# Kernel tuning notes

Measured on AMD Instinct MI355X. Metric: run time of the kernel, lower is better.

## Reference

```python
import jax, jax.numpy as jnp
import numpy as np

B, L, D = 2, 1024, 768
K = 64            # window_size
MLP_HIDDEN = 128
DIFF_STEPS = 1
EPS = 1e-8        # torch F.cosine_similarity eps


def setup_inputs() -> dict:
    key = jax.random.key(0)
    ks = jax.random.split(key, 7)
    x = jax.random.normal(ks[0], (B, L, D), dtype=jnp.float32)
    alpha = jnp.asarray(0.1, dtype=jnp.float32)
    pos_emb = jax.random.normal(ks[1], (K, D), dtype=jnp.float32) * 0.02
    w1 = jax.random.normal(ks[2], (2 * D, MLP_HIDDEN), dtype=jnp.float32) * 0.02
    b1 = jnp.zeros((MLP_HIDDEN,), dtype=jnp.float32)
    w2 = jax.random.normal(ks[3], (MLP_HIDDEN, D), dtype=jnp.float32) * 0.02
    b2 = jnp.zeros((D,), dtype=jnp.float32)
    return {"x": x, "alpha": alpha, "pos_emb": pos_emb,
            "w1": w1, "b1": b1, "w2": w2, "b2": b2}


def reference(x, alpha, pos_emb, w1, b1, w2, b2):
    Bx, Lx, Dx = x.shape
    W = Lx - K + 1  # number of sliding windows
    # gather indices for unfold(2, K, 1): window w covers positions [w, w+K)
    idx = jnp.arange(W)[:, None] + jnp.arange(K)[None, :]  # [W, K]

    x_curr = x
    first_pre_energy = jnp.asarray(0.0, jnp.float32)
    final_post_energy = jnp.asarray(0.0, jnp.float32)
    total_update_norm = jnp.asarray(0.0, jnp.float32)
    total_cos_sim = jnp.asarray(0.0, jnp.float32)

    for step in range(DIFF_STEPS):
        windows = x_curr[:, idx, :]                 # [B, W, K, D]
        context = windows[:, :, :-1, :]             # [B, W, K-1, D]
        current = windows[:, :, -1, :]              # [B, W, D]
        pe = jnp.broadcast_to(pos_emb[: K - 1], (Bx, W, K - 1, Dx))
        mlp_in = jnp.concatenate([context, pe], axis=-1)        # [B, W, K-1, 2D]
        h = jax.nn.relu(jnp.einsum('bwkc,ch->bwkh', mlp_in, w1) + b1)
        pred = jnp.einsum('bwkh,hd->bwkd', h, w2) + b2          # [B, W, K-1, D]
        deltas = current[:, :, None, :] - pred                  # [B, W, K-1, D]
        mean_delta = deltas.mean(axis=2)                        # [B, W, D]
        update = -(alpha * mean_delta)                          # [B, W, D]
        x_next = x_curr.at[:, K - 1:, :].add(update)

        pre_energy = (mean_delta ** 2).sum(axis=-1).mean()
        up_norm = jnp.linalg.norm(update, axis=-1).mean()
        a = current
        b = current + update
        na = jnp.maximum(jnp.linalg.norm(a, axis=-1), EPS)
        nb = jnp.maximum(jnp.linalg.norm(b, axis=-1), EPS)
        cos_sim = ((a * b).sum(axis=-1) / (na * nb)).mean()

        if step == 0:
            first_pre_energy = pre_energy
        total_update_norm = total_update_norm + up_norm
        total_cos_sim = total_cos_sim + cos_sim
        x_curr = x_next
        alpha_val = jax.lax.stop_gradient(alpha)  # mirrors .item() detach
        post_energy = (1.0 - alpha_val) ** 2 * pre_energy
        if step == DIFF_STEPS - 1:
            final_post_energy = post_energy

    return (x_curr,
            first_pre_energy,
            final_post_energy,
            total_update_norm / DIFF_STEPS,
            total_cos_sim / DIFF_STEPS)
```

## Files before the change

kernel.cpp:

```cpp
#include <hip/hip_runtime.h>

constexpr int Bn = 2;
constexpr int Ln = 1024;
constexpr int Dn = 768;
constexpr int Hn = 128;
constexpr int KM1 = 63;
constexpr int Wn = 961;
constexpr int RB = 8;
constexpr int WB = 8;
constexpr int WCHUNKS = (Wn + WB - 1) / WB;
constexpr int NROW = Bn * Wn;
constexpr float EPSf = 1e-8f;

__device__ __forceinline__ float4 f4l(const float* p) { return *reinterpret_cast<const float4*>(p); }
__device__ __forceinline__ void f4s(float* p, float4 v) { *reinterpret_cast<float4*>(p) = v; }
__device__ __forceinline__ float4 f4fma(float s, float4 w, float4 a) {
    a.x = fmaf(s, w.x, a.x); a.y = fmaf(s, w.y, a.y);
    a.z = fmaf(s, w.z, a.z); a.w = fmaf(s, w.w, a.w);
    return a;
}

__global__ __launch_bounds__(1024)
void k_gemm1(const float* __restrict__ x, const float* __restrict__ pos_emb,
             const float* __restrict__ w1, const float* __restrict__ b1,
             float* __restrict__ xw1, float* __restrict__ pew1,
             float* __restrict__ out)
{
    __shared__ float xs[RB * Dn];
    __shared__ float part[8 * RB * Hn];
    const int tid = threadIdx.x;
    const int h4 = tid & 31;
    const int is = (tid >> 5) & 3;
    const int ks = tid >> 7;
    const int blk = blockIdx.x;
    constexpr int NXB = (Bn * Ln) / RB;
    const bool isX = blk < NXB;
    const int peb = blk - NXB;

    const float* src = isX ? (x + blk * RB * Dn) : (pos_emb + peb * RB * Dn);
    const int nv = isX ? RB : min(RB, KM1 - peb * RB);

    for (int idx = tid; idx < nv * (Dn / 4); idx += 1024)
        ((float4*)xs)[idx] = ((const float4*)src)[idx];
    __syncthreads();

    if (isX) {
        const int r0 = blk * RB;
        if ((r0 & (Ln - 1)) < KM1) {
            for (int idx = tid; idx < RB * (Dn / 4); idx += 1024) {
                const int i = idx / (Dn / 4);
                const int r = r0 + i;
                if ((r & (Ln - 1)) < KM1)
                    ((float4*)out)[r * (Dn / 4) + (idx - i * (Dn / 4))] = ((const float4*)xs)[idx];
            }
        }
    }

    const int woff = isX ? 0 : Dn;
    const int i0 = is * 2;
    float4 acc0 = make_float4(0.f, 0.f, 0.f, 0.f);
    float4 acc1 = acc0;
    const int cbase = ks * (Dn / 8);
    for (int cc = 0; cc < Dn / 8; cc += 4) {
        const int c = cbase + cc;
        const float* wp = w1 + (woff + c) * Hn + 4 * h4;
        const float4 wv0 = f4l(wp);
        const float4 wv1 = f4l(wp + Hn);
        const float4 wv2 = f4l(wp + 2 * Hn);
        const float4 wv3 = f4l(wp + 3 * Hn);
        const float4 x0 = ((const float4*)xs)[(i0 * Dn + c) >> 2];
        const float4 x1 = ((const float4*)xs)[((i0 + 1) * Dn + c) >> 2];
        acc0 = f4fma(x0.x, wv0, acc0); acc0 = f4fma(x0.y, wv1, acc0);
        acc0 = f4fma(x0.z, wv2, acc0); acc0 = f4fma(x0.w, wv3, acc0);
        acc1 = f4fma(x1.x, wv0, acc1); acc1 = f4fma(x1.y, wv1, acc1);
        acc1 = f4fma(x1.z, wv2, acc1); acc1 = f4fma(x1.w, wv3, acc1);
    }
    ((float4*)part)[((ks * RB + i0) * Hn + 4 * h4) >> 2] = acc0;
    ((float4*)part)[((ks * RB + i0 + 1) * Hn + 4 * h4) >> 2] = acc1;
    __syncthreads();

    const int oi = tid >> 7;
    const int oh = tid & 127;
    float s = 0.f;
    #pragma unroll
    for (int k2 = 0; k2 < 8; ++k2)
        s += part[(k2 * RB + oi) * Hn + oh];
    if (isX) {
        xw1[(blk * RB + oi) * Hn + oh] = s;
    } else if (oi < nv) {
        pew1[(peb * RB + oi) * Hn + oh] = s + b1[oh];
    }
}

__global__ __launch_bounds__(256)
void k_hbar(const float* __restrict__ xw1, const float* __restrict__ pew1,
            float* __restrict__ hbar)
{
    __shared__ float4 prt[8][32];
    const int tid = threadIdx.x;
    const int h4 = tid & 31;
    const int kg = tid >> 5;
    const int b = blockIdx.x / Wn;
    const int w = blockIdx.x - b * Wn;
    const float* xp = xw1 + (b * Ln + w + kg * 8) * Hn + 4 * h4;
    const float* pp = pew1 + (kg * 8) * Hn + 4 * h4;
    const int nk = (kg == 7) ? 7 : 8;
    float4 s = make_float4(0.f, 0.f, 0.f, 0.f);
    for (int j = 0; j < nk; ++j) {
        const float4 xv = f4l(xp + j * Hn);
        const float4 pv = f4l(pp + j * Hn);
        s.x += fmaxf(xv.x + pv.x, 0.f);
        s.y += fmaxf(xv.y + pv.y, 0.f);
        s.z += fmaxf(xv.z + pv.z, 0.f);
        s.w += fmaxf(xv.w + pv.w, 0.f);
    }
    prt[kg][h4] = s;
    __syncthreads();
    if (tid < 32) {
        float4 t = prt[0][tid];
        #pragma unroll
        for (int k = 1; k < 8; ++k) {
            const float4 u = prt[k][tid];
            t.x += u.x; t.y += u.y; t.z += u.z; t.w += u.w;
        }
        const float sc = 1.0f / 63.0f;
        t.x *= sc; t.y *= sc; t.z *= sc; t.w *= sc;
        ((float4*)(hbar + blockIdx.x * Hn))[tid] = t;
    }
}

__global__ __launch_bounds__(256)
void k_gemm2(const float* __restrict__ x, const float* __restrict__ alpha_p,
             const float* __restrict__ w2, const float* __restrict__ b2,
             const float* __restrict__ hbar, float* __restrict__ out,
             float* __restrict__ partial)
{
    __shared__ float hsm[WB * Hn];
    __shared__ float4 red[4 * WB * 64];
    const int tid = threadIdx.x;
    int bid = blockIdx.x;
    const int dc = bid % 3; bid /= 3;
    const int chunk = bid % WCHUNKS;
    const int b = bid / WCHUNKS;
    const int w0 = chunk * WB;
    const int wcount = min(WB, Wn - w0);
    const float alpha = alpha_p[0];

    {
        const float4 z = make_float4(0.f, 0.f, 0.f, 0.f);
        ((float4*)hsm)[tid] = (tid < wcount * (Hn / 4))
            ? ((const float4*)(hbar + (b * Wn + w0) * Hn))[tid] : z;
    }
    __syncthreads();

    const int d4 = tid & 63;
    const int hs = tid >> 6;
    const int d = dc * 256 + d4 * 4;

    float4 acc[WB];
    #pragma unroll
    for (int w = 0; w < WB; ++w) acc[w] = make_float4(0.f, 0.f, 0.f, 0.f);
    const int h0 = hs * 32;
    for (int hh = 0; hh < 32; ++hh) {
        const int h = h0 + hh;
        const float4 wv = f4l(w2 + h * Dn + d);
        #pragma unroll
        for (int w = 0; w < WB; ++w)
            acc[w] = f4fma(hsm[w * Hn + h], wv, acc[w]);
    }
    #pragma unroll
    for (int w = 0; w < WB; ++w)
        red[(hs * WB + w) * 64 + d4] = acc[w];
    __syncthreads();

    const int wloc = tid >> 5;
    float4 pp = make_float4(0.f, 0.f, 0.f, 0.f);
    if (wloc < wcount) {
        const int rowoff = (b * Ln + w0 + wloc + KM1) * Dn + dc * 256;
        #pragma unroll
        for (int j = 0; j < 2; ++j) {
            const int dp = (2 * tid + j) & 63;
            float4 sum = red[wloc * 64 + dp];
            #pragma unroll
            for (int k = 1; k < 4; ++k) {
                const float4 u = red[(k * WB + wloc) * 64 + dp];
                sum.x += u.x; sum.y += u.y; sum.z += u.z; sum.w += u.w;
            }
            const float4 bb = f4l(b2 + dc * 256 + dp * 4);
            const float4 xv = f4l(x + rowoff + dp * 4);
            float4 md;
            md.x = xv.x - (sum.x + bb.x);
            md.y = xv.y - (sum.y + bb.y);
            md.z = xv.z - (sum.z + bb.z);
            md.w = xv.w - (sum.w + bb.w);
            float4 nb;
            nb.x = fmaf(-alpha, md.x, xv.x);
            nb.y = fmaf(-alpha, md.y, xv.y);
            nb.z = fmaf(-alpha, md.z, xv.z);
            nb.w = fmaf(-alpha, md.w, xv.w);
            f4s(out + rowoff + dp * 4, nb);
            pp.x += md.x * md.x + md.y * md.y + md.z * md.z + md.w * md.w;
            pp.y += xv.x * xv.x + xv.y * xv.y + xv.z * xv.z + xv.w * xv.w;
            pp.z += xv.x * nb.x + xv.y * nb.y + xv.z * nb.z + xv.w * nb.w;
            pp.w += nb.x * nb.x + nb.y * nb.y + nb.z * nb.z + nb.w * nb.w;
        }
    }
    #pragma unroll
    for (int off = 16; off > 0; off >>= 1) {
        pp.x += __shfl_xor(pp.x, off);
        pp.y += __shfl_xor(pp.y, off);
        pp.z += __shfl_xor(pp.z, off);
        pp.w += __shfl_xor(pp.w, off);
    }
    if (((tid & 31) == 0) && wloc < wcount)
        f4s(partial + (dc * NROW + b * Wn + w0 + wloc) * 4, pp);
}

__global__ __launch_bounds__(1024)
void k_final(const float* __restrict__ partial, const float* __restrict__ alpha_p,
             float* __restrict__ out)
{
    __shared__ float sred[16][3];
    const int tid = threadIdx.x;
    float se = 0.f, sn = 0.f, sc = 0.f;
    for (int r = tid; r < NROW; r += 1024) {
        const float4 v0 = ((const float4*)partial)[r];
        const float4 v1 = ((const float4*)partial)[NROW + r];
        const float4 v2 = ((const float4*)partial)[2 * NROW + r];
        const float sq = v0.x + v1.x + v2.x;
        const float aa = v0.y + v1.y + v2.y;
        const float ab = v0.z + v1.z + v2.z;
        const float bb = v0.w + v1.w + v2.w;
        se += sq;
        sn += sqrtf(sq);
        sc += ab / (fmaxf(sqrtf(aa), EPSf) * fmaxf(sqrtf(bb), EPSf));
    }
    #pragma unroll
    for (int off = 32; off > 0; off >>= 1) {
        se += __shfl_down(se, off);
        sn += __shfl_down(sn, off);
        sc += __shfl_down(sc, off);
    }
    const int wv = tid >> 6, lane = tid & 63;
    if (lane == 0) { sred[wv][0] = se; sred[wv][1] = sn; sred[wv][2] = sc; }
    __syncthreads();
    if (tid == 0) {
        float te = 0.f, tn = 0.f, tc = 0.f;
        #pragma unroll
        for (int i = 0; i < 16; ++i) {
            te += sred[i][0]; tn += sred[i][1]; tc += sred[i][2];
        }
        const float alpha = alpha_p[0];
        const float inv = 1.0f / (float)NROW;
        const float pre = te * inv;
        const float om = 1.0f - alpha;
        const int base = Bn * Ln * Dn;
        out[base + 0] = pre;
        out[base + 1] = om * om * pre;
        out[base + 2] = alpha * tn * inv;
        out[base + 3] = tc * inv;
    }
}

extern "C" void kernel_launch(void* const* d_in, const int* in_sizes, int n_in,
                              void* d_out, int out_size, void* d_ws, size_t ws_size,
                              hipStream_t stream)
{
    const float* x       = (const float*)d_in[0];
    const float* alpha_p = (const float*)d_in[1];
    const float* pos_emb = (const float*)d_in[2];
    const float* w1      = (const float*)d_in[3];
    const float* b1      = (const float*)d_in[4];
    const float* w2      = (const float*)d_in[5];
    const float* b2      = (const float*)d_in[6];
    float* out = (float*)d_out;

    float* xw1     = (float*)d_ws;
    float* pew1    = xw1 + Bn * Ln * Hn;
    float* hbar    = pew1 + KM1 * Hn;
    float* partial = hbar + NROW * Hn;

    const int nblkA = (Bn * Ln) / RB + (KM1 + RB - 1) / RB;
    k_gemm1<<<nblkA, 1024, 0, stream>>>(x, pos_emb, w1, b1, xw1, pew1, out);
    k_hbar<<<NROW, 256, 0, stream>>>(xw1, pew1, hbar);
    k_gemm2<<<Bn * WCHUNKS * 3, 256, 0, stream>>>(x, alpha_p, w2, b2, hbar, out, partial);
    k_final<<<1, 1024, 0, stream>>>(partial, alpha_p, out);
}
```

Before: 112.1 us.

## Fuse hbar window averaging into gemm2 and retile gemm1 to 4-row blocks

Drops the separate k_hbar kernel. Each gemm2 block now loads the needed xw1 rows into shared memory and computes the relu-mean hidden vectors for its 8 windows before the second matmul, which removes a launch and the hbar round trip through global memory. Because gemm2 blocks are split three ways along D, the hbar work is repeated three times per window chunk. gemm1 is also retiled to 4 rows per block with 512 threads and a 16-way K split, which doubles its block count. The pew1 reads in the fused loop go straight to global memory.

```diff
diff --git a/kernel.cpp b/kernel.cpp
--- a/kernel.cpp
+++ b/kernel.cpp
@@ -6,7 +6,7 @@
 constexpr int Hn = 128;
 constexpr int KM1 = 63;
 constexpr int Wn = 961;
-constexpr int RB = 8;
+constexpr int RB = 4;
 constexpr int WB = 8;
 constexpr int WCHUNKS = (Wn + WB - 1) / WB;
 constexpr int NROW = Bn * Wn;
@@ -20,18 +20,17 @@
     return a;
 }
 
-__global__ __launch_bounds__(1024)
+__global__ __launch_bounds__(512)
 void k_gemm1(const float* __restrict__ x, const float* __restrict__ pos_emb,
              const float* __restrict__ w1, const float* __restrict__ b1,
              float* __restrict__ xw1, float* __restrict__ pew1,
              float* __restrict__ out)
 {
     __shared__ float xs[RB * Dn];
-    __shared__ float part[8 * RB * Hn];
+    __shared__ float part[16 * RB * Hn];
     const int tid = threadIdx.x;
     const int h4 = tid & 31;
-    const int is = (tid >> 5) & 3;
-    const int ks = tid >> 7;
+    const int ks = tid >> 5;
     const int blk = blockIdx.x;
     constexpr int NXB = (Bn * Ln) / RB;
     const bool isX = blk < NXB;
@@ -40,14 +39,14 @@
     const float* src = isX ? (x + blk * RB * Dn) : (pos_emb + peb * RB * Dn);
     const int nv = isX ? RB : min(RB, KM1 - peb * RB);
 
-    for (int idx = tid; idx < nv * (Dn / 4); idx += 1024)
+    for (int idx = tid; idx < nv * (Dn / 4); idx += 512)
         ((float4*)xs)[idx] = ((const float4*)src)[idx];
     __syncthreads();
 
     if (isX) {
         const int r0 = blk * RB;
         if ((r0 & (Ln - 1)) < KM1) {
-            for (int idx = tid; idx < RB * (Dn / 4); idx += 1024) {
+            for (int idx = tid; idx < RB * (Dn / 4); idx += 512) {
                 const int i = idx / (Dn / 4);
                 const int r = r0 + i;
                 if ((r & (Ln - 1)) < KM1)
@@ -57,33 +56,40 @@
     }
 
     const int woff = isX ? 0 : Dn;
-    const int i0 = is * 2;
     float4 acc0 = make_float4(0.f, 0.f, 0.f, 0.f);
-    float4 acc1 = acc0;
-    const int cbase = ks * (Dn / 8);
-    for (int cc = 0; cc < Dn / 8; cc += 4) {
+    float4 acc1 = acc0, acc2 = acc0, acc3 = acc0;
+    const int cbase = ks * 48;
+    for (int cc = 0; cc < 48; cc += 4) {
         const int c = cbase + cc;
         const float* wp = w1 + (woff + c) * Hn + 4 * h4;
         const float4 wv0 = f4l(wp);
         const float4 wv1 = f4l(wp + Hn);
         const float4 wv2 = f4l(wp + 2 * Hn);
         const float4 wv3 = f4l(wp + 3 * Hn);
-        const float4 x0 = ((const float4*)xs)[(i0 * Dn + c) >> 2];
-        const float4 x1 = ((const float4*)xs)[((i0 + 1) * Dn + c) >> 2];
+        const float4 x0 = ((const float4*)xs)[(0 * Dn + c) >> 2];
+        const float4 x1 = ((const float4*)xs)[(1 * Dn + c) >> 2];
+        const float4 x2 = ((const float4*)xs)[(2 * Dn + c) >> 2];
+        const float4 x3 = ((const float4*)xs)[(3 * Dn + c) >> 2];
         acc0 = f4fma(x0.x, wv0, acc0); acc0 = f4fma(x0.y, wv1, acc0);
         acc0 = f4fma(x0.z, wv2, acc0); acc0 = f4fma(x0.w, wv3, acc0);
         acc1 = f4fma(x1.x, wv0, acc1); acc1 = f4fma(x1.y, wv1, acc1);
         acc1 = f4fma(x1.z, wv2, acc1); acc1 = f4fma(x1.w, wv3, acc1);
-    }
-    ((float4*)part)[((ks * RB + i0) * Hn + 4 * h4) >> 2] = acc0;
-    ((float4*)part)[((ks * RB + i0 + 1) * Hn + 4 * h4) >> 2] = acc1;
+        acc2 = f4fma(x2.x, wv0, acc2); acc2 = f4fma(x2.y, wv1, acc2);
+        acc2 = f4fma(x2.z, wv2, acc2); acc2 = f4fma(x2.w, wv3, acc2);
+        acc3 = f4fma(x3.x, wv0, acc3); acc3 = f4fma(x3.y, wv1, acc3);
+        acc3 = f4fma(x3.z, wv2, acc3); acc3 = f4fma(x3.w, wv3, acc3);
+    }
+    ((float4*)part)[((ks * RB + 0) * Hn + 4 * h4) >> 2] = acc0;
+    ((float4*)part)[((ks * RB + 1) * Hn + 4 * h4) >> 2] = acc1;
+    ((float4*)part)[((ks * RB + 2) * Hn + 4 * h4) >> 2] = acc2;
+    ((float4*)part)[((ks * RB + 3) * Hn + 4 * h4) >> 2] = acc3;
     __syncthreads();
 
     const int oi = tid >> 7;
     const int oh = tid & 127;
     float s = 0.f;
     #pragma unroll
-    for (int k2 = 0; k2 < 8; ++k2)
+    for (int k2 = 0; k2 < 16; ++k2)
         s += part[(k2 * RB + oi) * Hn + oh];
     if (isX) {
         xw1[(blk * RB + oi) * Hn + oh] = s;
@@ -93,48 +99,12 @@
 }
 
 __global__ __launch_bounds__(256)
-void k_hbar(const float* __restrict__ xw1, const float* __restrict__ pew1,
-            float* __restrict__ hbar)
-{
-    __shared__ float4 prt[8][32];
-    const int tid = threadIdx.x;
-    const int h4 = tid & 31;
-    const int kg = tid >> 5;
-    const int b = blockIdx.x / Wn;
-    const int w = blockIdx.x - b * Wn;
-    const float* xp = xw1 + (b * Ln + w + kg * 8) * Hn + 4 * h4;
-    const float* pp = pew1 + (kg * 8) * Hn + 4 * h4;
-    const int nk = (kg == 7) ? 7 : 8;
-    float4 s = make_float4(0.f, 0.f, 0.f, 0.f);
-    for (int j = 0; j < nk; ++j) {
-        const float4 xv = f4l(xp + j * Hn);
-        const float4 pv = f4l(pp + j * Hn);
-        s.x += fmaxf(xv.x + pv.x, 0.f);
-        s.y += fmaxf(xv.y + pv.y, 0.f);
-        s.z += fmaxf(xv.z + pv.z, 0.f);
-        s.w += fmaxf(xv.w + pv.w, 0.f);
-    }
-    prt[kg][h4] = s;
-    __syncthreads();
-    if (tid < 32) {
-        float4 t = prt[0][tid];
-        #pragma unroll
-        for (int k = 1; k < 8; ++k) {
-            const float4 u = prt[k][tid];
-            t.x += u.x; t.y += u.y; t.z += u.z; t.w += u.w;
-        }
-        const float sc = 1.0f / 63.0f;
-        t.x *= sc; t.y *= sc; t.z *= sc; t.w *= sc;
-        ((float4*)(hbar + blockIdx.x * Hn))[tid] = t;
-    }
-}
-
-__global__ __launch_bounds__(256)
-void k_gemm2(const float* __restrict__ x, const float* __restrict__ alpha_p,
+void k_fused(const float* __restrict__ x, const float* __restrict__ alpha_p,
              const float* __restrict__ w2, const float* __restrict__ b2,
-             const float* __restrict__ hbar, float* __restrict__ out,
-             float* __restrict__ partial)
-{
+             const float* __restrict__ xw1, const float* __restrict__ pew1,
+             float* __restrict__ out, float* __restrict__ partial)
+{
+    __shared__ float xsl[(WB + KM1 - 1) * Hn];
     __shared__ float hsm[WB * Hn];
     __shared__ float4 red[4 * WB * 64];
     const int tid = threadIdx.x;
@@ -144,22 +114,42 @@
     const int b = bid / WCHUNKS;
     const int w0 = chunk * WB;
     const int wcount = min(WB, Wn - w0);
+    const int nrows = wcount + KM1 - 1;
     const float alpha = alpha_p[0];
 
     {
-        const float4 z = make_float4(0.f, 0.f, 0.f, 0.f);
-        ((float4*)hsm)[tid] = (tid < wcount * (Hn / 4))
-            ? ((const float4*)(hbar + (b * Wn + w0) * Hn))[tid] : z;
+        const float4* src = (const float4*)(xw1 + (b * Ln + w0) * Hn);
+        for (int idx = tid; idx < nrows * (Hn / 4); idx += 256)
+            ((float4*)xsl)[idx] = src[idx];
+    }
+    __syncthreads();
+
+    {
+        const int w = tid >> 5;
+        const int h4 = tid & 31;
+        float4 s = make_float4(0.f, 0.f, 0.f, 0.f);
+        const float* pp = pew1 + 4 * h4;
+        #pragma unroll 7
+        for (int k = 0; k < KM1; ++k) {
+            const float4 xv = ((const float4*)xsl)[((w + k) * Hn + 4 * h4) >> 2];
+            const float4 pv = f4l(pp + k * Hn);
+            s.x += fmaxf(xv.x + pv.x, 0.f);
+            s.y += fmaxf(xv.y + pv.y, 0.f);
+            s.z += fmaxf(xv.z + pv.z, 0.f);
+            s.w += fmaxf(xv.w + pv.w, 0.f);
+        }
+        const float sc = 1.0f / 63.0f;
+        s.x *= sc; s.y *= sc; s.z *= sc; s.w *= sc;
+        ((float4*)hsm)[(w * Hn + 4 * h4) >> 2] = s;
     }
     __syncthreads();
 
     const int d4 = tid & 63;
     const int hs = tid >> 6;
+    float4 acc[WB];
+    #pragma unroll
+    for (int w = 0; w < WB; ++w) acc[w] = make_float4(0.f, 0.f, 0.f, 0.f);
     const int d = dc * 256 + d4 * 4;
-
-    float4 acc[WB];
-    #pragma unroll
-    for (int w = 0; w < WB; ++w) acc[w] = make_float4(0.f, 0.f, 0.f, 0.f);
     const int h0 = hs * 32;
     for (int hh = 0; hh < 32; ++hh) {
         const int h = h0 + hh;
@@ -277,12 +267,10 @@
 
     float* xw1     = (float*)d_ws;
     float* pew1    = xw1 + Bn * Ln * Hn;
-    float* hbar    = pew1 + KM1 * Hn;
-    float* partial = hbar + NROW * Hn;
+    float* partial = pew1 + KM1 * Hn;
 
     const int nblkA = (Bn * Ln) / RB + (KM1 + RB - 1) / RB;
-    k_gemm1<<<nblkA, 1024, 0, stream>>>(x, pos_emb, w1, b1, xw1, pew1, out);
-    k_hbar<<<NROW, 256, 0, stream>>>(xw1, pew1, hbar);
-    k_gemm2<<<Bn * WCHUNKS * 3, 256, 0, stream>>>(x, alpha_p, w2, b2, hbar, out, partial);
+    k_gemm1<<<nblkA, 512, 0, stream>>>(x, pos_emb, w1, b1, xw1, pew1, out);
+    k_fused<<<Bn * WCHUNKS * 3, 256, 0, stream>>>(x, alpha_p, w2, b2, xw1, pew1, out, partial);
     k_final<<<1, 1024, 0, stream>>>(partial, alpha_p, out);
 }
```

Result: faster. 107.9 us (-3.8%).

## Fuse four kernels into one cooperative persistent kernel with grid syncs

Applied to the files above, without the earlier changes.

Replaces the four separate launches with a single cooperative kernel of 256 blocks that runs the GEMM1, window-mean, GEMM2 and final-reduction phases separated by grid.sync(). Each phase is retiled for 512 threads: GEMM1 takes 8 rows per block with shuffle-based split-K, hbar handles 8 windows per unit, and GEMM2 handles 16 windows per unit. This removes inter-kernel launch gaps and the many tiny hbar blocks. In exchange it adds grid-wide barrier cost and leaves fewer blocks than the earlier grids, and it falls back to four separate launches if the cooperative launch fails.

```diff
diff --git a/kernel.cpp b/kernel.cpp
--- a/kernel.cpp
+++ b/kernel.cpp
@@ -1,4 +1,6 @@
 #include <hip/hip_runtime.h>
+#include <hip/hip_cooperative_groups.h>
+namespace cg = cooperative_groups;
 
 constexpr int Bn = 2;
 constexpr int Ln = 1024;
@@ -6,11 +8,21 @@
 constexpr int Hn = 128;
 constexpr int KM1 = 63;
 constexpr int Wn = 961;
-constexpr int RB = 8;
-constexpr int WB = 8;
-constexpr int WCHUNKS = (Wn + WB - 1) / WB;
 constexpr int NROW = Bn * Wn;
+constexpr int GRID = 256;
+constexpr int THR = 512;
 constexpr float EPSf = 1e-8f;
+
+constexpr int RB1 = 8;
+constexpr int PSTR = 132;
+constexpr int WB2 = 8;
+constexpr int CH2 = (Wn + WB2 - 1) / WB2;
+constexpr int U2 = Bn * CH2;
+constexpr int WB3 = 16;
+constexpr int CH3 = (Wn + WB3 - 1) / WB3;
+constexpr int U3 = Bn * CH3 * 3;
+
+constexpr int POOLF = RB1 * Dn + 4 * RB1 * PSTR;
 
 __device__ __forceinline__ float4 f4l(const float* p) { return *reinterpret_cast<const float4*>(p); }
 __device__ __forceinline__ void f4s(float* p, float4 v) { *reinterpret_cast<float4*>(p) = v; }
@@ -20,237 +32,293 @@
     return a;
 }
 
-__global__ __launch_bounds__(1024)
-void k_gemm1(const float* __restrict__ x, const float* __restrict__ pos_emb,
-             const float* __restrict__ w1, const float* __restrict__ b1,
-             float* __restrict__ xw1, float* __restrict__ pew1,
-             float* __restrict__ out)
-{
-    __shared__ float xs[RB * Dn];
-    __shared__ float part[8 * RB * Hn];
-    const int tid = threadIdx.x;
-    const int h4 = tid & 31;
-    const int is = (tid >> 5) & 3;
-    const int ks = tid >> 7;
-    const int blk = blockIdx.x;
-    constexpr int NXB = (Bn * Ln) / RB;
-    const bool isX = blk < NXB;
-    const int peb = blk - NXB;
-
-    const float* src = isX ? (x + blk * RB * Dn) : (pos_emb + peb * RB * Dn);
-    const int nv = isX ? RB : min(RB, KM1 - peb * RB);
-
-    for (int idx = tid; idx < nv * (Dn / 4); idx += 1024)
-        ((float4*)xs)[idx] = ((const float4*)src)[idx];
-    __syncthreads();
-
-    if (isX) {
-        const int r0 = blk * RB;
-        if ((r0 & (Ln - 1)) < KM1) {
-            for (int idx = tid; idx < RB * (Dn / 4); idx += 1024) {
-                const int i = idx / (Dn / 4);
-                const int r = r0 + i;
-                if ((r & (Ln - 1)) < KM1)
-                    ((float4*)out)[r * (Dn / 4) + (idx - i * (Dn / 4))] = ((const float4*)xs)[idx];
-            }
-        }
-    }
-
-    const int woff = isX ? 0 : Dn;
-    const int i0 = is * 2;
-    float4 acc0 = make_float4(0.f, 0.f, 0.f, 0.f);
-    float4 acc1 = acc0;
-    const int cbase = ks * (Dn / 8);
-    for (int cc = 0; cc < Dn / 8; cc += 4) {
-        const int c = cbase + cc;
-        const float* wp = w1 + (woff + c) * Hn + 4 * h4;
+__device__ void phase1(float* xs, float* part,
+                       const float* __restrict__ x, const float* __restrict__ pos_emb,
+                       const float* __restrict__ w1, const float* __restrict__ b1,
+                       float* __restrict__ xw1, float* __restrict__ pew1,
+                       float* __restrict__ out, int blk, int tid)
+{
+    const int r0 = blk * RB1;
+    for (int idx = tid; idx < RB1 * (Dn / 4); idx += THR)
+        ((float4*)xs)[idx] = ((const float4*)(x + r0 * Dn))[idx];
+    __syncthreads();
+
+    if ((blk & 127) < 8) {
+        for (int idx = tid; idx < RB1 * (Dn / 4); idx += THR) {
+            const int i = idx / (Dn / 4);
+            const int r = r0 + i;
+            if ((r & (Ln - 1)) < KM1)
+                ((float4*)out)[r * (Dn / 4) + idx - i * (Dn / 4)] = ((const float4*)xs)[idx];
+        }
+    }
+
+    const int hh = tid >> 8;
+    const int t = tid & 255;
+    const int h4 = t & 15;
+    const int s = (t >> 4) & 15;
+    const int quad = t >> 6;
+    const int hbase = hh * 64 + 4 * h4;
+
+    float4 acc[RB1];
+    #pragma unroll
+    for (int r = 0; r < RB1; ++r) acc[r] = make_float4(0.f, 0.f, 0.f, 0.f);
+    #pragma unroll
+    for (int j = 0; j < 12; ++j) {
+        const int c = 4 * s + 64 * j;
+        const float* wp = w1 + c * Hn + hbase;
         const float4 wv0 = f4l(wp);
         const float4 wv1 = f4l(wp + Hn);
         const float4 wv2 = f4l(wp + 2 * Hn);
         const float4 wv3 = f4l(wp + 3 * Hn);
-        const float4 x0 = ((const float4*)xs)[(i0 * Dn + c) >> 2];
-        const float4 x1 = ((const float4*)xs)[((i0 + 1) * Dn + c) >> 2];
-        acc0 = f4fma(x0.x, wv0, acc0); acc0 = f4fma(x0.y, wv1, acc0);
-        acc0 = f4fma(x0.z, wv2, acc0); acc0 = f4fma(x0.w, wv3, acc0);
-        acc1 = f4fma(x1.x, wv0, acc1); acc1 = f4fma(x1.y, wv1, acc1);
-        acc1 = f4fma(x1.z, wv2, acc1); acc1 = f4fma(x1.w, wv3, acc1);
-    }
-    ((float4*)part)[((ks * RB + i0) * Hn + 4 * h4) >> 2] = acc0;
-    ((float4*)part)[((ks * RB + i0 + 1) * Hn + 4 * h4) >> 2] = acc1;
-    __syncthreads();
-
-    const int oi = tid >> 7;
-    const int oh = tid & 127;
-    float s = 0.f;
-    #pragma unroll
-    for (int k2 = 0; k2 < 8; ++k2)
-        s += part[(k2 * RB + oi) * Hn + oh];
-    if (isX) {
-        xw1[(blk * RB + oi) * Hn + oh] = s;
-    } else if (oi < nv) {
-        pew1[(peb * RB + oi) * Hn + oh] = s + b1[oh];
-    }
-}
-
-__global__ __launch_bounds__(256)
-void k_hbar(const float* __restrict__ xw1, const float* __restrict__ pew1,
-            float* __restrict__ hbar)
-{
-    __shared__ float4 prt[8][32];
-    const int tid = threadIdx.x;
+        #pragma unroll
+        for (int r = 0; r < RB1; ++r) {
+            const float4 xv = ((const float4*)xs)[r * (Dn / 4) + s + 16 * j];
+            acc[r] = f4fma(xv.x, wv0, acc[r]);
+            acc[r] = f4fma(xv.y, wv1, acc[r]);
+            acc[r] = f4fma(xv.z, wv2, acc[r]);
+            acc[r] = f4fma(xv.w, wv3, acc[r]);
+        }
+    }
+    #pragma unroll
+    for (int r = 0; r < RB1; ++r) {
+        acc[r].x += __shfl_xor(acc[r].x, 16); acc[r].y += __shfl_xor(acc[r].y, 16);
+        acc[r].z += __shfl_xor(acc[r].z, 16); acc[r].w += __shfl_xor(acc[r].w, 16);
+        acc[r].x += __shfl_xor(acc[r].x, 32); acc[r].y += __shfl_xor(acc[r].y, 32);
+        acc[r].z += __shfl_xor(acc[r].z, 32); acc[r].w += __shfl_xor(acc[r].w, 32);
+    }
+    if ((t & 48) == 0) {
+        #pragma unroll
+        for (int r = 0; r < RB1; ++r)
+            f4s(part + (quad * RB1 + r) * PSTR + hbase, acc[r]);
+    }
+    __syncthreads();
+    for (int o = tid; o < RB1 * Hn; o += THR) {
+        const int r = o >> 7, hl = o & 127;
+        float sum = 0.f;
+        #pragma unroll
+        for (int q = 0; q < 4; ++q) sum += part[(q * RB1 + r) * PSTR + hl];
+        xw1[(r0 + r) * Hn + hl] = sum;
+    }
+
+    if (blk < 16) {
+        const int pr0 = blk * 4;
+        const int nv = min(4, KM1 - pr0);
+        __syncthreads();
+        for (int idx = tid; idx < nv * (Dn / 4); idx += THR)
+            ((float4*)xs)[idx] = ((const float4*)(pos_emb + pr0 * Dn))[idx];
+        __syncthreads();
+        float4 pa[4];
+        #pragma unroll
+        for (int r = 0; r < 4; ++r) pa[r] = make_float4(0.f, 0.f, 0.f, 0.f);
+        #pragma unroll
+        for (int j = 0; j < 12; ++j) {
+            const int c = 4 * s + 64 * j;
+            const float* wp = w1 + (Dn + c) * Hn + hbase;
+            const float4 wv0 = f4l(wp);
+            const float4 wv1 = f4l(wp + Hn);
+            const float4 wv2 = f4l(wp + 2 * Hn);
+            const float4 wv3 = f4l(wp + 3 * Hn);
+            #pragma unroll
+            for (int r = 0; r < 4; ++r) {
+                const float4 xv = ((const float4*)xs)[r * (Dn / 4) + s + 16 * j];
+                pa[r] = f4fma(xv.x, wv0, pa[r]);
+                pa[r] = f4fma(xv.y, wv1, pa[r]);
+                pa[r] = f4fma(xv.z, wv2, pa[r]);
+                pa[r] = f4fma(xv.w, wv3, pa[r]);
+            }
+        }
+        #pragma unroll
+        for (int r = 0; r < 4; ++r) {
+            pa[r].x += __shfl_xor(pa[r].x, 16); pa[r].y += __shfl_xor(pa[r].y, 16);
+            pa[r].z += __shfl_xor(pa[r].z, 16); pa[r].w += __shfl_xor(pa[r].w, 16);
+            pa[r].x += __shfl_xor(pa[r].x, 32); pa[r].y += __shfl_xor(pa[r].y, 32);
+            pa[r].z += __shfl_xor(pa[r].z, 32); pa[r].w += __shfl_xor(pa[r].w, 32);
+        }
+        if ((t & 48) == 0) {
+            #pragma unroll
+            for (int r = 0; r < 4; ++r)
+                f4s(part + (quad * RB1 + r) * PSTR + hbase, pa[r]);
+        }
+        __syncthreads();
+        {
+            const int r = tid >> 7, hl = tid & 127;
+            if (r < nv) {
+                float sum = 0.f;
+                #pragma unroll
+                for (int q = 0; q < 4; ++q) sum += part[(q * RB1 + r) * PSTR + hl];
+                pew1[(pr0 + r) * Hn + hl] = sum + b1[hl];
+            }
+        }
+    }
+}
+
+__device__ void phase2(float* kred, const float* __restrict__ xw1,
+                       const float* __restrict__ pew1, float* __restrict__ hbar,
+                       int u, int tid)
+{
+    const int b = u / CH2;
+    const int chunk = u % CH2;
+    const int w0 = chunk * WB2;
+    const int wcount = min(WB2, Wn - w0);
     const int h4 = tid & 31;
     const int kg = tid >> 5;
-    const int b = blockIdx.x / Wn;
-    const int w = blockIdx.x - b * Wn;
-    const float* xp = xw1 + (b * Ln + w + kg * 8) * Hn + 4 * h4;
-    const float* pp = pew1 + (kg * 8) * Hn + 4 * h4;
-    const int nk = (kg == 7) ? 7 : 8;
-    float4 s = make_float4(0.f, 0.f, 0.f, 0.f);
-    for (int j = 0; j < nk; ++j) {
-        const float4 xv = f4l(xp + j * Hn);
-        const float4 pv = f4l(pp + j * Hn);
-        s.x += fmaxf(xv.x + pv.x, 0.f);
-        s.y += fmaxf(xv.y + pv.y, 0.f);
-        s.z += fmaxf(xv.z + pv.z, 0.f);
-        s.w += fmaxf(xv.w + pv.w, 0.f);
-    }
-    prt[kg][h4] = s;
-    __syncthreads();
-    if (tid < 32) {
-        float4 t = prt[0][tid];
-        #pragma unroll
-        for (int k = 1; k < 8; ++k) {
-            const float4 u = prt[k][tid];
-            t.x += u.x; t.y += u.y; t.z += u.z; t.w += u.w;
-        }
-        const float sc = 1.0f / 63.0f;
-        t.x *= sc; t.y *= sc; t.z *= sc; t.w *= sc;
-        ((float4*)(hbar + blockIdx.x * Hn))[tid] = t;
-    }
-}
-
-__global__ __launch_bounds__(256)
-void k_gemm2(const float* __restrict__ x, const float* __restrict__ alpha_p,
-             const float* __restrict__ w2, const float* __restrict__ b2,
-             const float* __restrict__ hbar, float* __restrict__ out,
-             float* __restrict__ partial)
-{
-    __shared__ float hsm[WB * Hn];
-    __shared__ float4 red[4 * WB * 64];
-    const int tid = threadIdx.x;
-    int bid = blockIdx.x;
-    const int dc = bid % 3; bid /= 3;
-    const int chunk = bid % WCHUNKS;
-    const int b = bid / WCHUNKS;
-    const int w0 = chunk * WB;
-    const int wcount = min(WB, Wn - w0);
+    float4 sw[WB2];
+    #pragma unroll
+    for (int w = 0; w < WB2; ++w) sw[w] = make_float4(0.f, 0.f, 0.f, 0.f);
+    for (int k = kg; k < KM1; k += 16) {
+        const float4 pv = f4l(pew1 + k * Hn + 4 * h4);
+        #pragma unroll
+        for (int w = 0; w < WB2; ++w) {
+            int rr = w0 + w + k; rr = rr < Ln ? rr : (Ln - 1);
+            const float4 xv = f4l(xw1 + (b * Ln + rr) * Hn + 4 * h4);
+            sw[w].x += fmaxf(xv.x + pv.x, 0.f);
+            sw[w].y += fmaxf(xv.y + pv.y, 0.f);
+            sw[w].z += fmaxf(xv.z + pv.z, 0.f);
+            sw[w].w += fmaxf(xv.w + pv.w, 0.f);
+        }
+    }
+    #pragma unroll
+    for (int w = 0; w < WB2; ++w) {
+        sw[w].x += __shfl_xor(sw[w].x, 32);
+        sw[w].y += __shfl_xor(sw[w].y, 32);
+        sw[w].z += __shfl_xor(sw[w].z, 32);
+        sw[w].w += __shfl_xor(sw[w].w, 32);
+    }
+    const int kgE = tid >> 6;
+    if ((tid & 63) < 32) {
+        #pragma unroll
+        for (int w = 0; w < WB2; ++w)
+            ((float4*)kred)[(kgE * WB2 + w) * 32 + h4] = sw[w];
+    }
+    __syncthreads();
+    const float scl = 1.0f / 63.0f;
+    for (int o = tid; o < WB2 * Hn; o += THR) {
+        const int w = o >> 7, h = o & 127;
+        if (w < wcount) {
+            float tsum = 0.f;
+            #pragma unroll
+            for (int g = 0; g < 8; ++g)
+                tsum += kred[(g * WB2 + w) * 128 + h];
+            hbar[(b * Wn + w0 + w) * Hn + h] = tsum * scl;
+        }
+    }
+}
+
+__device__ void phase3(float* hsm, const float* __restrict__ x,
+                       const float* __restrict__ alpha_p, const float* __restrict__ w2,
+                       const float* __restrict__ b2, const float* __restrict__ hbar,
+                       float* __restrict__ out, float* __restrict__ partial,
+                       int u, int tid)
+{
+    const int dc = u % 3;
+    const int rest = u / 3;
+    const int b = rest / CH3;
+    const int chunk = rest % CH3;
+    const int w0 = chunk * WB3;
+    const int wcount = min(WB3, Wn - w0);
     const float alpha = alpha_p[0];
 
+    __syncthreads();
     {
-        const float4 z = make_float4(0.f, 0.f, 0.f, 0.f);
-        ((float4*)hsm)[tid] = (tid < wcount * (Hn / 4))
-            ? ((const float4*)(hbar + (b * Wn + w0) * Hn))[tid] : z;
-    }
-    __syncthreads();
-
+        const int idx = tid;
+        const int w = idx >> 5;
+        ((float4*)hsm)[idx] = (w < wcount)
+            ? ((const float4*)(hbar + (b * Wn + w0) * Hn))[idx]
+            : make_float4(0.f, 0.f, 0.f, 0.f);
+    }
+    __syncthreads();
+
+    const int wg = tid >> 6;
     const int d4 = tid & 63;
-    const int hs = tid >> 6;
     const int d = dc * 256 + d4 * 4;
-
-    float4 acc[WB];
-    #pragma unroll
-    for (int w = 0; w < WB; ++w) acc[w] = make_float4(0.f, 0.f, 0.f, 0.f);
-    const int h0 = hs * 32;
-    for (int hh = 0; hh < 32; ++hh) {
-        const int h = h0 + hh;
-        const float4 wv = f4l(w2 + h * Dn + d);
-        #pragma unroll
-        for (int w = 0; w < WB; ++w)
-            acc[w] = f4fma(hsm[w * Hn + h], wv, acc[w]);
-    }
-    #pragma unroll
-    for (int w = 0; w < WB; ++w)
-        red[(hs * WB + w) * 64 + d4] = acc[w];
-    __syncthreads();
-
-    const int wloc = tid >> 5;
-    float4 pp = make_float4(0.f, 0.f, 0.f, 0.f);
-    if (wloc < wcount) {
-        const int rowoff = (b * Ln + w0 + wloc + KM1) * Dn + dc * 256;
-        #pragma unroll
-        for (int j = 0; j < 2; ++j) {
-            const int dp = (2 * tid + j) & 63;
-            float4 sum = red[wloc * 64 + dp];
-            #pragma unroll
-            for (int k = 1; k < 4; ++k) {
-                const float4 u = red[(k * WB + wloc) * 64 + dp];
-                sum.x += u.x; sum.y += u.y; sum.z += u.z; sum.w += u.w;
-            }
-            const float4 bb = f4l(b2 + dc * 256 + dp * 4);
-            const float4 xv = f4l(x + rowoff + dp * 4);
+    const int w0r = (wg * 2) * 32, w1r = (wg * 2 + 1) * 32;
+    float4 acc0 = make_float4(0.f, 0.f, 0.f, 0.f);
+    float4 acc1 = acc0;
+    for (int hi = 0; hi < 32; ++hi) {
+        const float* wp = w2 + (4 * hi) * Dn + d;
+        const float4 wv0 = f4l(wp);
+        const float4 wv1 = f4l(wp + Dn);
+        const float4 wv2 = f4l(wp + 2 * Dn);
+        const float4 wv3 = f4l(wp + 3 * Dn);
+        const float4 h0 = ((const float4*)hsm)[w0r + hi];
+        const float4 h1 = ((const float4*)hsm)[w1r + hi];
+        acc0 = f4fma(h0.x, wv0, acc0); acc0 = f4fma(h0.y, wv1, acc0);
+        acc0 = f4fma(h0.z, wv2, acc0); acc0 = f4fma(h0.w, wv3, acc0);
+        acc1 = f4fma(h1.x, wv0, acc1); acc1 = f4fma(h1.y, wv1, acc1);
+        acc1 = f4fma(h1.z, wv2, acc1); acc1 = f4fma(h1.w, wv3, acc1);
+    }
+    const float4 bb = f4l(b2 + d);
+    #pragma unroll
+    for (int j = 0; j < 2; ++j) {
+        const int w = wg * 2 + j;
+        float4 pp = make_float4(0.f, 0.f, 0.f, 0.f);
+        if (w < wcount) {
+            const float4 sum0 = (j == 0) ? acc0 : acc1;
+            const int row = b * Ln + w0 + w + KM1;
+            const int off = row * Dn + d;
+            const float4 xv = f4l(x + off);
             float4 md;
-            md.x = xv.x - (sum.x + bb.x);
-            md.y = xv.y - (sum.y + bb.y);
-            md.z = xv.z - (sum.z + bb.z);
-            md.w = xv.w - (sum.w + bb.w);
+            md.x = xv.x - (sum0.x + bb.x);
+            md.y = xv.y - (sum0.y + bb.y);
+            md.z = xv.z - (sum0.z + bb.z);
+            md.w = xv.w - (sum0.w + bb.w);
             float4 nb;
             nb.x = fmaf(-alpha, md.x, xv.x);
             nb.y = fmaf(-alpha, md.y, xv.y);
             nb.z = fmaf(-alpha, md.z, xv.z);
             nb.w = fmaf(-alpha, md.w, xv.w);
-            f4s(out + rowoff + dp * 4, nb);
-            pp.x += md.x * md.x + md.y * md.y + md.z * md.z + md.w * md.w;
-            pp.y += xv.x * xv.x + xv.y * xv.y + xv.z * xv.z + xv.w * xv.w;
-            pp.z += xv.x * nb.x + xv.y * nb.y + xv.z * nb.z + xv.w * nb.w;
-            pp.w += nb.x * nb.x + nb.y * nb.y + nb.z * nb.z + nb.w * nb.w;
-        }
-    }
-    #pragma unroll
-    for (int off = 16; off > 0; off >>= 1) {
-        pp.x += __shfl_xor(pp.x, off);
-        pp.y += __shfl_xor(pp.y, off);
-        pp.z += __shfl_xor(pp.z, off);
-        pp.w += __shfl_xor(pp.w, off);
-    }
-    if (((tid & 31) == 0) && wloc < wcount)
-        f4s(partial + (dc * NROW + b * Wn + w0 + wloc) * 4, pp);
-}
-
-__global__ __launch_bounds__(1024)
-void k_final(const float* __restrict__ partial, const float* __restrict__ alpha_p,
-             float* __restrict__ out)
-{
-    __shared__ float sred[16][3];
-    const int tid = threadIdx.x;
+            f4s(out + off, nb);
+            pp.x = md.x * md.x + md.y * md.y + md.z * md.z + md.w * md.w;
+            pp.y = xv.x * xv.x + xv.y * xv.y + xv.z * xv.z + xv.w * xv.w;
+            pp.z = xv.x * nb.x + xv.y * nb.y + xv.z * nb.z + xv.w * nb.w;
+            pp.w = nb.x * nb.x + nb.y * nb.y + nb.z * nb.z + nb.w * nb.w;
+        }
+        #pragma unroll
+        for (int o = 32; o > 0; o >>= 1) {
+            pp.x += __shfl_xor(pp.x, o);
+            pp.y += __shfl_xor(pp.y, o);
+            pp.z += __shfl_xor(pp.z, o);
+            pp.w += __shfl_xor(pp.w, o);
+        }
+        if ((tid & 63) == 0 && w < wcount)
+            f4s(partial + (dc * NROW + b * Wn + w0 + w) * 4, pp);
+    }
+}
+
+__device__ void phase4(float* fin, const float* __restrict__ partial,
+                       const float* __restrict__ alpha_p, float* __restrict__ out,
+                       int tid)
+{
+    const float alpha = alpha_p[0];
     float se = 0.f, sn = 0.f, sc = 0.f;
-    for (int r = tid; r < NROW; r += 1024) {
-        const float4 v0 = ((const float4*)partial)[r];
-        const float4 v1 = ((const float4*)partial)[NROW + r];
-        const float4 v2 = ((const float4*)partial)[2 * NROW + r];
+    const float4* pf = (const float4*)partial;
+    for (int r = tid; r < NROW; r += THR) {
+        const float4 v0 = pf[r];
+        const float4 v1 = pf[NROW + r];
+        const float4 v2 = pf[2 * NROW + r];
         const float sq = v0.x + v1.x + v2.x;
         const float aa = v0.y + v1.y + v2.y;
         const float ab = v0.z + v1.z + v2.z;
-        const float bb = v0.w + v1.w + v2.w;
+        const float bbs = v0.w + v1.w + v2.w;
         se += sq;
         sn += sqrtf(sq);
-        sc += ab / (fmaxf(sqrtf(aa), EPSf) * fmaxf(sqrtf(bb), EPSf));
-    }
-    #pragma unroll
-    for (int off = 32; off > 0; off >>= 1) {
-        se += __shfl_down(se, off);
-        sn += __shfl_down(sn, off);
-        sc += __shfl_down(sc, off);
+        sc += ab / (fmaxf(sqrtf(aa), EPSf) * fmaxf(sqrtf(bbs), EPSf));
+    }
+    #pragma unroll
+    for (int o = 32; o > 0; o >>= 1) {
+        se += __shfl_down(se, o);
+        sn += __shfl_down(sn, o);
+        sc += __shfl_down(sc, o);
     }
     const int wv = tid >> 6, lane = tid & 63;
-    if (lane == 0) { sred[wv][0] = se; sred[wv][1] = sn; sred[wv][2] = sc; }
+    if (lane == 0) { fin[wv * 3 + 0] = se; fin[wv * 3 + 1] = sn; fin[wv * 3 + 2] = sc; }
     __syncthreads();
     if (tid == 0) {
         float te = 0.f, tn = 0.f, tc = 0.f;
         #pragma unroll
-        for (int i = 0; i < 16; ++i) {
-            te += sred[i][0]; tn += sred[i][1]; tc += sred[i][2];
-        }
-        const float alpha = alpha_p[0];
+        for (int i = 0; i < 8; ++i) {
+            te += fin[i * 3 + 0]; tn += fin[i * 3 + 1]; tc += fin[i * 3 + 2];
+        }
         const float inv = 1.0f / (float)NROW;
         const float pre = te * inv;
         const float om = 1.0f - alpha;
@@ -262,6 +330,58 @@
     }
 }
 
+__global__ __launch_bounds__(THR)
+void k_all(const float* __restrict__ x, const float* __restrict__ alpha_p,
+           const float* __restrict__ pos_emb, const float* __restrict__ w1,
+           const float* __restrict__ b1, const float* __restrict__ w2,
+           const float* __restrict__ b2, float* __restrict__ out,
+           float* __restrict__ xw1, float* __restrict__ pew1,
+           float* __restrict__ hbar, float* __restrict__ partial)
+{
+    __shared__ __align__(16) float pool[POOLF];
+    cg::grid_group grid = cg::this_grid();
+    const int blk = blockIdx.x;
+    const int tid = threadIdx.x;
+
+    phase1(pool, pool + RB1 * Dn, x, pos_emb, w1, b1, xw1, pew1, out, blk, tid);
+    grid.sync();
+    if (blk < U2) phase2(pool, xw1, pew1, hbar, blk, tid);
+    grid.sync();
+    phase3(pool, x, alpha_p, w2, b2, hbar, out, partial, blk, tid);
+    if (blk + GRID < U3)
+        phase3(pool, x, alpha_p, w2, b2, hbar, out, partial, blk + GRID, tid);
+    grid.sync();
+    if (blk == 0) phase4(pool, partial, alpha_p, out, tid);
+}
+
+__global__ __launch_bounds__(THR)
+void k_p1(const float* x, const float* pos_emb, const float* w1, const float* b1,
+          float* xw1, float* pew1, float* out)
+{
+    __shared__ __align__(16) float pool[POOLF];
+    phase1(pool, pool + RB1 * Dn, x, pos_emb, w1, b1, xw1, pew1, out,
+           blockIdx.x, threadIdx.x);
+}
+__global__ __launch_bounds__(THR)
+void k_p2(const float* xw1, const float* pew1, float* hbar)
+{
+    __shared__ __align__(16) float pool[8192];
+    phase2(pool, xw1, pew1, hbar, blockIdx.x, threadIdx.x);
+}
+__global__ __launch_bounds__(THR)
+void k_p3(const float* x, const float* alpha_p, const float* w2, const float* b2,
+          const float* hbar, float* out, float* partial)
+{
+    __shared__ __align__(16) float pool[2048];
+    phase3(pool, x, alpha_p, w2, b2, hbar, out, partial, blockIdx.x, threadIdx.x);
+}
+__global__ __launch_bounds__(THR)
+void k_p4(const float* partial, const float* alpha_p, float* out)
+{
+    __shared__ __align__(16) float pool[32];
+    phase4(pool, partial, alpha_p, out, threadIdx.x);
+}
+
 extern "C" void kernel_launch(void* const* d_in, const int* in_sizes, int n_in,
                               void* d_out, int out_size, void* d_ws, size_t ws_size,
                               hipStream_t stream)
@@ -277,12 +397,18 @@
 
     float* xw1     = (float*)d_ws;
     float* pew1    = xw1 + Bn * Ln * Hn;
-    float* hbar    = pew1 + KM1 * Hn;
+    float* hbar    = pew1 + 64 * Hn;
     float* partial = hbar + NROW * Hn;
 
-    const int nblkA = (Bn * Ln) / RB + (KM1 + RB - 1) / RB;
-    k_gemm1<<<nblkA, 1024, 0, stream>>>(x, pos_emb, w1, b1, xw1, pew1, out);
-    k_hbar<<<NROW, 256, 0, stream>>>(xw1, pew1, hbar);
-    k_gemm2<<<Bn * WCHUNKS * 3, 256, 0, stream>>>(x, alpha_p, w2, b2, hbar, out, partial);
-    k_final<<<1, 1024, 0, stream>>>(partial, alpha_p, out);
-}
+    void* args[] = { (void*)&x, (void*)&alpha_p, (void*)&pos_emb, (void*)&w1,
+                     (void*)&b1, (void*)&w2, (void*)&b2, (void*)&out,
+                     (void*)&xw1, (void*)&pew1, (void*)&hbar, (void*)&partial };
+    hipError_t err = hipLaunchCooperativeKernel((const void*)k_all, dim3(GRID),
+                                                dim3(THR), args, 0, stream);
+    if (err != hipSuccess) {
+        k_p1<<<GRID, THR, 0, stream>>>(x, pos_emb, w1, b1, xw1, pew1, out);
+        k_p2<<<U2, THR, 0, stream>>>(xw1, pew1, hbar);
+        k_p3<<<U3, THR, 0, stream>>>(x, alpha_p, w2, b2, hbar, out, partial);
+        k_p4<<<1, THR, 0, stream>>>(partial, alpha_p, out);
+    }
+}
```

After: 217.7 us. +94.2%, slower.
